# Kernel optimization log

Measured on AMD Instinct MI355X. Metric: run time of the kernel, lower is better.

The kernel has to match this reference:

```python
import jax, jax.numpy as jnp
import numpy as np

B, L, D_IN = 4, 2048, 80
D, H, DFF, WIN = 128, 16, 128, 64
DH = D // H
BN_EPS = 1e-5


def sinusoidal_positional_encoding(l, d, dtype):
    # Faithful to source: pos_j = 10000 ** (j / d) (exponent j/d, not 2j/d)
    n = d // 2 + (d % 2 == 1)
    pos_i = jnp.arange(l, dtype=dtype)[:, None]                  # [L,1]
    pos_j = jnp.power(jnp.asarray(10000.0, dtype), jnp.arange(n, dtype=dtype) / d)  # [n]
    ang = pos_i / pos_j                                          # [L,n]
    pos = jnp.stack([jnp.sin(ang), jnp.cos(ang)], axis=-1).reshape(l, -1)
    return pos[:, :d]                                            # [L,D]


def local_window_disallowed_mask(l, win):
    # Source: mask starts as ones (True = disallowed), zeros only strictly
    i = jnp.arange(l)
    diff = jnp.abs(i[:, None] - i[None, :])
    allowed = (diff >= 1) & (diff <= win)
    return ~allowed                                              # [L,L] bool, True = masked


def setup_inputs() -> dict:
    key = jax.random.key(0)
    ks = jax.random.split(key, 17)
    s = 0.05  # weight scale for numerical stability
    return {
        "x": jax.random.normal(ks[0], (B, L, D_IN), jnp.float32),
        "conv_w": jax.random.normal(ks[1], (D, D_IN), jnp.float32) * s,
        "conv_b": jax.random.normal(ks[2], (D,), jnp.float32) * s,
        "bn_g": jax.random.uniform(ks[3], (D,), jnp.float32, 0.5, 1.5),
        "bn_b": jax.random.normal(ks[4], (D,), jnp.float32) * s,
        "bn_rm": jax.random.normal(ks[5], (D,), jnp.float32) * s,
        "bn_rv": jax.random.uniform(ks[6], (D,), jnp.float32, 0.5, 1.5),
        "in_proj_w": jax.random.normal(ks[7], (3 * D, D), jnp.float32) * s,
        "in_proj_b": jax.random.normal(ks[8], (3 * D,), jnp.float32) * s,
        "out_w": jax.random.normal(ks[9], (D, D), jnp.float32) * s,
        "out_b": jax.random.normal(ks[10], (D,), jnp.float32) * s,
        "ff_w1": jax.random.normal(ks[11], (DFF, D), jnp.float32) * s,
        "ff_b1": jax.random.normal(ks[12], (DFF,), jnp.float32) * s,
        "ff_w2": jax.random.normal(ks[13], (D, DFF), jnp.float32) * s,
        "ff_b2": jax.random.normal(ks[14], (D,), jnp.float32) * s,
        "fc_w": jax.random.normal(ks[15], (D_IN, D), jnp.float32) * s,
        "fc_b": jax.random.normal(ks[16], (D_IN,), jnp.float32) * s,
    }


def _forward(x, conv_w, conv_b, bn_g, bn_b, bn_rm, bn_rv,
             in_proj_w, in_proj_b, out_w, out_b,
             ff_w1, ff_b1, ff_w2, ff_b2, fc_w, fc_b):
    b, l, _ = x.shape
    dt = x.dtype
    # Conv1d(kernel=1) + ReLU + BatchNorm1d (eval mode, running stats)
    h = jax.nn.relu(jnp.einsum('bli,oi->blo', x, conv_w) + conv_b)     # [B,L,D]
    h = (h - bn_rm) * (bn_g * jax.lax.rsqrt(bn_rv + BN_EPS)) + bn_b
    # positional encoding
    h = h + sinusoidal_positional_encoding(l, D, dt)
    # MultiheadAttention (torch semantics: joint in_proj, scaled dot, out_proj)
    qkv = jnp.einsum('bld,ed->ble', h, in_proj_w) + in_proj_b          # [B,L,3D]
    q, k, v = jnp.split(qkv, 3, axis=-1)
    q = q.reshape(b, l, H, DH).transpose(0, 2, 1, 3)                   # [B,H,L,dh]
    k = k.reshape(b, l, H, DH).transpose(0, 2, 1, 3)
    v = v.reshape(b, l, H, DH).transpose(0, 2, 1, 3)
    scores = jnp.einsum('bhqd,bhkd->bhqk', q, k) / jnp.sqrt(jnp.asarray(DH, dt))
    mask = local_window_disallowed_mask(l, WIN)                        # True = masked
    scores = jnp.where(mask, jnp.finfo(dt).min, scores)
    attn = jax.nn.softmax(scores, axis=-1)                             # [B,H,L,L]
    ctx = jnp.einsum('bhqk,bhkd->bhqd', attn, v)
    ctx = ctx.transpose(0, 2, 1, 3).reshape(b, l, D)
    attn_out = jnp.einsum('bld,od->blo', ctx, out_w) + out_b           # [B,L,D]
    # FFN (no residual in source)
    f = jax.nn.relu(jnp.einsum('bld,fd->blf', attn_out, ff_w1) + ff_b1)
    f = jnp.einsum('blf,df->bld', f, ff_w2) + ff_b2                    # [B,L,D]
    # final head
    return jnp.einsum('bld,od->blo', f, fc_w) + fc_b                   # [B,L,80]


def reference(x, conv_w, conv_b, bn_g, bn_b, bn_rm, bn_rv,
              in_proj_w, in_proj_b, out_w, out_b,
              ff_w1, ff_b1, ff_w2, ff_b2, fc_w, fc_b):
    return _forward(x, conv_w, conv_b, bn_g, bn_b, bn_rm, bn_rv,
                    in_proj_w, in_proj_b, out_w, out_b,
                    ff_w1, ff_b1, ff_w2, ff_b2, fc_w, fc_b)
```

## Files before the change

kernel.cpp:

```cpp
#include <hip/hip_runtime.h>
#include <math.h>

constexpr int B_ = 4, L_ = 2048, DIN = 80, D_ = 128, H_ = 16, DH = 8;
constexpr int T_ = B_ * L_;
constexpr int LDX = T_;

__device__ float g_xT  [DIN * T_];
__device__ float g_posT[D_ * L_];
__device__ float g_h   [D_ * T_];
__device__ float g_qkv [3 * D_ * T_];
__device__ float g_ctx [D_ * T_];
__device__ float g_f1  [D_ * T_];
__device__ float g_WconvT[DIN * D_];
__device__ float g_WqkvT [D_ * 3 * D_];
__device__ float g_Wf1T  [D_ * D_];
__device__ float g_WfcT  [D_ * D_];
__device__ float g_bf1   [D_];
__device__ float g_bfc   [D_];

__global__ __launch_bounds__(256) void prep_kernel(
        const float* __restrict__ x,
        const float* __restrict__ conv_w,
        const float* __restrict__ in_proj_w,
        const float* __restrict__ out_w,  const float* __restrict__ out_b,
        const float* __restrict__ ff_w1,  const float* __restrict__ ff_b1,
        const float* __restrict__ ff_w2,  const float* __restrict__ ff_b2,
        const float* __restrict__ fc_w,   const float* __restrict__ fc_b) {
    __shared__ float smem[80 * 65];
    int bid = blockIdx.x, tid = threadIdx.x;

    if (bid < 128) {
        int t0 = bid * 64;
        for (int i = tid; i < 64 * 80; i += 256) {
            int t = i / 80, k = i - t * 80;
            smem[k * 65 + t] = x[(size_t)t0 * 80 + i];
        }
        __syncthreads();
        for (int i = tid; i < 80 * 64; i += 256) {
            int k = i >> 6, tt = i & 63;
            g_xT[(size_t)k * T_ + t0 + tt] = smem[k * 65 + tt];
        }
        return;
    }
    if (bid < 640) {
        int idx = (bid - 128) * 256 + tid;
        int l = idx >> 6, j = idx & 63;
        float inv = __expf((float)j * (-9.210340371976184f / 128.0f));
        float ang = (float)l * inv;
        g_posT[(2 * j) * L_ + l]     = sinf(ang);
        g_posT[(2 * j + 1) * L_ + l] = cosf(ang);
        return;
    }
    if (bid < 680) {
        int e = (bid - 640) * 256 + tid;
        int o = e / 80, k = e - o * 80;
        g_WconvT[k * D_ + o] = conv_w[e];
        return;
    }
    if (bid < 872) {
        int e = (bid - 680) * 256 + tid;
        int o = e >> 7, k = e & 127;
        g_WqkvT[k * (3 * D_) + o] = in_proj_w[e];
        return;
    }
    float* rowbuf = smem;
    float* red = smem + 256;
    if (bid < 936) {
        int sub = tid >> 7, k = tid & 127;
        int f = (bid - 872) * 2 + sub;
        rowbuf[sub * 128 + k] = ff_w1[f * 128 + k];
        __syncthreads();
        float acc = 0.f;
#pragma unroll 8
        for (int o = 0; o < 128; o++)
            acc = fmaf(rowbuf[sub * 128 + o], out_w[o * 128 + k], acc);
        g_Wf1T[k * 128 + f] = acc;
        red[tid] = rowbuf[sub * 128 + k] * out_b[k];
        __syncthreads();
        for (int s = 64; s > 0; s >>= 1) {
            if (k < s) red[tid] += red[tid + s];
            __syncthreads();
        }
        if (k == 0) g_bf1[f] = red[sub * 128] + ff_b1[f];
        return;
    }
    {
        int sub = tid >> 7, k = tid & 127;
        int o = (bid - 936) * 2 + sub;
        rowbuf[sub * 128 + k] = (o < 80) ? fc_w[o * 128 + k] : 0.f;
        __syncthreads();
        float acc = 0.f;
#pragma unroll 8
        for (int d = 0; d < 128; d++)
            acc = fmaf(rowbuf[sub * 128 + d], ff_w2[d * 128 + k], acc);
        g_WfcT[k * 128 + o] = acc;
        red[tid] = rowbuf[sub * 128 + k] * ff_b2[k];
        __syncthreads();
        for (int s = 64; s > 0; s >>= 1) {
            if (k < s) red[tid] += red[tid + s];
            __syncthreads();
        }
        if (k == 0) g_bfc[o] = (o < 80) ? (red[sub * 128] + fc_b[o]) : 0.f;
        return;
    }
}

template <int K, int BK, int BN, int LDW, int EPI>
__global__ __launch_bounds__(256) void gemm_kernel(
        const float* __restrict__ X, const float* __restrict__ Wt,
        const float* __restrict__ bias,
        const float* __restrict__ bg, const float* __restrict__ bb,
        const float* __restrict__ brm, const float* __restrict__ brv,
        float* __restrict__ Y) {
    constexpr int TN = BN / 16;
    __shared__ float Xs[BK][64];
    __shared__ float Ws[BK][BN];
    int tid = threadIdx.x;
    int t0 = blockIdx.x * 64;
    int cb = blockIdx.y * BN;
    int tc = tid & 15, tr = tid >> 4;

    float acc[4][TN] = {};
    for (int kc = 0; kc < K; kc += BK) {
        for (int i = tid; i < BK * 16; i += 256) {
            int k = i >> 4, f = i & 15;
            *(float4*)&Xs[k][f * 4] =
                *(const float4*)&X[(size_t)(kc + k) * LDX + t0 + f * 4];
        }
        for (int i = tid; i < BK * (BN / 4); i += 256) {
            int k = i / (BN / 4), f = i - k * (BN / 4);
            *(float4*)&Ws[k][f * 4] =
                *(const float4*)&Wt[(size_t)(kc + k) * LDW + cb + f * 4];
        }
        __syncthreads();
#pragma unroll 4
        for (int k = 0; k < BK; ++k) {
            float4 a = *(float4*)&Xs[k][tr * 4];
            float av[4] = {a.x, a.y, a.z, a.w};
            float wv[TN];
#pragma unroll
            for (int jj = 0; jj < TN; jj++) wv[jj] = Ws[k][tc * TN + jj];
#pragma unroll
            for (int i = 0; i < 4; i++)
#pragma unroll
                for (int jj = 0; jj < TN; jj++)
                    acc[i][jj] = fmaf(av[i], wv[jj], acc[i][jj]);
        }
        __syncthreads();
    }

    if (EPI == 4) {
#pragma unroll
        for (int jj = 0; jj < TN; jj++) {
            int c = cb + tc * TN + jj;
            if (c < 80) {
                float bv = bias[c];
#pragma unroll
                for (int i = 0; i < 4; i++) {
                    int t = t0 + tr * 4 + i;
                    Y[(size_t)t * 80 + c] = acc[i][jj] + bv;
                }
            }
        }
        return;
    }
#pragma unroll
    for (int jj = 0; jj < TN; jj++) {
        int c = cb + tc * TN + jj;
        float bv = bias[c];
        float vs[4];
#pragma unroll
        for (int i = 0; i < 4; i++) {
            float v = acc[i][jj] + bv;
            if (EPI == 1) v = fmaxf(v, 0.0f);
            if (EPI == 2) {
                v = fmaxf(v, 0.0f);
                v = (v - brm[c]) * (bg[c] * rsqrtf(brv[c] + 1e-5f)) + bb[c];
                v += g_posT[c * L_ + ((t0 & 2047) + tr * 4 + i)];
            }
            vs[i] = v;
        }
        *(float4*)&Y[(size_t)c * LDX + t0 + tr * 4] = *(float4*)vs;
    }
}

__global__ __launch_bounds__(256) void attn_kernel() {
    __shared__ float4 SK[2][2][324];
    __shared__ float4 SV[2][2][324];
    int bh = blockIdx.x;
    int qb = blockIdx.y * 512;
    int b = bh >> 4, h = bh & 15;
    int tb = b * L_;
    int tid = threadIdx.x;
    int jbase = qb - 64;

    for (int c16 = 0; c16 < 16; c16++) {
        int d = c16 & 7;
        int ch = ((c16 < 8) ? D_ : 2 * D_) + h * 8 + d;
        const float* src = g_qkv + (size_t)ch * LDX + tb;
        float4* base4 = ((c16 < 8) ? &SK[0][0][0] : &SV[0][0][0]) + (d >> 2) * 324;
        for (int s = tid; s < 641; s += 256) {
            int j = jbase + s;
            float v = ((unsigned)j < (unsigned)L_) ? src[j] : 0.f;
            ((float*)(base4 + (s & 1) * 648 + (s >> 1)))[d & 3] = v;
        }
    }
    __syncthreads();

    const float sc = 0.35355339059327373f;
    int q0 = qb + 2 * tid;
    float qa[8], qc[8];
#pragma unroll
    for (int d = 0; d < 8; d++) {
        qa[d] = g_qkv[(size_t)(h * 8 + d) * LDX + tb + q0] * sc;
        qc[d] = g_qkv[(size_t)(h * 8 + d) * LDX + tb + q0 + 1] * sc;
    }
    float l0 = 0.f, l1 = 0.f;
    float A0[8] = {}, A1[8] = {};
    int j00 = jbase + 2 * tid;

#pragma unroll 2
    for (int it = 0; it <= 129; it++) {
        int pp = it & 1, idx = tid + (it >> 1);
        float4 ka = SK[pp][0][idx], kb2 = SK[pp][1][idx];
        float kv[8] = {ka.x, ka.y, ka.z, ka.w, kb2.x, kb2.y, kb2.z, kb2.w};
        float s0 = 0.f, s1 = 0.f;
#pragma unroll
        for (int d = 0; d < 8; d++) {
            s0 = fmaf(qa[d], kv[d], s0);
            s1 = fmaf(qc[d], kv[d], s1);
        }
        bool jv = (unsigned)(j00 + it) < (unsigned)L_;
        float w0 = (jv && it != 64 && it <= 128) ? __expf(s0) : 0.f;
        float w1 = (jv && it != 65 && it >= 1)  ? __expf(s1) : 0.f;
        l0 += w0; l1 += w1;
        float4 va = SV[pp][0][idx], vb2 = SV[pp][1][idx];
        float vv[8] = {va.x, va.y, va.z, va.w, vb2.x, vb2.y, vb2.z, vb2.w};
#pragma unroll
        for (int d = 0; d < 8; d++) {
            A0[d] = fmaf(w0, vv[d], A0[d]);
            A1[d] = fmaf(w1, vv[d], A1[d]);
        }
    }
    float i0 = 1.f / l0, i1 = 1.f / l1;
    int base = tb + q0;
#pragma unroll
    for (int d = 0; d < 8; d++) {
        g_ctx[(size_t)(h * 8 + d) * LDX + base]     = A0[d] * i0;
        g_ctx[(size_t)(h * 8 + d) * LDX + base + 1] = A1[d] * i1;
    }
}

extern "C" void kernel_launch(void* const* d_in, const int* in_sizes, int n_in,
                              void* d_out, int out_size, void* d_ws, size_t ws_size,
                              hipStream_t stream) {
    const float* x         = (const float*)d_in[0];
    const float* conv_w    = (const float*)d_in[1];
    const float* conv_b    = (const float*)d_in[2];
    const float* bn_g      = (const float*)d_in[3];
    const float* bn_b      = (const float*)d_in[4];
    const float* bn_rm     = (const float*)d_in[5];
    const float* bn_rv     = (const float*)d_in[6];
    const float* in_proj_w = (const float*)d_in[7];
    const float* in_proj_b = (const float*)d_in[8];
    const float* out_w     = (const float*)d_in[9];
    const float* out_b     = (const float*)d_in[10];
    const float* ff_w1     = (const float*)d_in[11];
    const float* ff_b1     = (const float*)d_in[12];
    const float* ff_w2     = (const float*)d_in[13];
    const float* ff_b2     = (const float*)d_in[14];
    const float* fc_w      = (const float*)d_in[15];
    const float* fc_b      = (const float*)d_in[16];

    float *p_xT, *p_h, *p_qkv, *p_ctx, *p_f1;
    float *p_WconvT, *p_WqkvT, *p_Wf1T, *p_WfcT, *p_bf1, *p_bfc;
    hipGetSymbolAddress((void**)&p_xT,     HIP_SYMBOL(g_xT));
    hipGetSymbolAddress((void**)&p_h,      HIP_SYMBOL(g_h));
    hipGetSymbolAddress((void**)&p_qkv,    HIP_SYMBOL(g_qkv));
    hipGetSymbolAddress((void**)&p_ctx,    HIP_SYMBOL(g_ctx));
    hipGetSymbolAddress((void**)&p_f1,     HIP_SYMBOL(g_f1));
    hipGetSymbolAddress((void**)&p_WconvT, HIP_SYMBOL(g_WconvT));
    hipGetSymbolAddress((void**)&p_WqkvT,  HIP_SYMBOL(g_WqkvT));
    hipGetSymbolAddress((void**)&p_Wf1T,   HIP_SYMBOL(g_Wf1T));
    hipGetSymbolAddress((void**)&p_WfcT,   HIP_SYMBOL(g_WfcT));
    hipGetSymbolAddress((void**)&p_bf1,    HIP_SYMBOL(g_bf1));
    hipGetSymbolAddress((void**)&p_bfc,    HIP_SYMBOL(g_bfc));

    prep_kernel<<<1000, 256, 0, stream>>>(x, conv_w, in_proj_w, out_w, out_b,
                                          ff_w1, ff_b1, ff_w2, ff_b2, fc_w, fc_b);

    gemm_kernel<80, 80, 32, 128, 2><<<dim3(128, 4), 256, 0, stream>>>(
        p_xT, p_WconvT, conv_b, bn_g, bn_b, bn_rm, bn_rv, p_h);

    gemm_kernel<128, 64, 64, 384, 0><<<dim3(128, 6), 256, 0, stream>>>(
        p_h, p_WqkvT, in_proj_b, nullptr, nullptr, nullptr, nullptr, p_qkv);

    attn_kernel<<<dim3(64, 4), 256, 0, stream>>>();

    gemm_kernel<128, 128, 32, 128, 1><<<dim3(128, 4), 256, 0, stream>>>(
        p_ctx, p_Wf1T, p_bf1, nullptr, nullptr, nullptr, nullptr, p_f1);

    gemm_kernel<128, 128, 32, 128, 4><<<dim3(128, 3), 256, 0, stream>>>(
        p_f1, p_WfcT, p_bfc, nullptr, nullptr, nullptr, nullptr, (float*)d_out);
}
```

Baseline: 167.6 us.

## Fuse FFN and output head GEMMs, add dedicated QKV kernel

Merges the two final GEMMs (ff1 with ReLU, then the fc head) into one kernel that keeps the intermediate activations in shared memory, so the g_f1 buffer is never written to or read back from global memory. The QKV projection moves to a specialised kernel with an 8x4 per-thread tile and vectorised weight loads. The conv GEMM tile width doubles to 64 so it launches half as many blocks, and the shared weight read becomes a float4 load when TN is 4. The fused kernel launches only 256 blocks with heavy shared-memory use, which may limit occupancy.

```diff
diff --git a/kernel.cpp b/kernel.cpp
--- a/kernel.cpp
+++ b/kernel.cpp
@@ -1,8 +1,9 @@
 #include <hip/hip_runtime.h>
 #include <math.h>
 
-constexpr int B_ = 4, L_ = 2048, DIN = 80, D_ = 128, H_ = 16, DH = 8;
-constexpr int T_ = B_ * L_;
+constexpr int L_ = 2048, D_ = 128, H_ = 16;
+constexpr int T_ = 8192;
+constexpr int DIN = 80;
 constexpr int LDX = T_;
 
 __device__ float g_xT  [DIN * T_];
@@ -10,7 +11,6 @@
 __device__ float g_h   [D_ * T_];
 __device__ float g_qkv [3 * D_ * T_];
 __device__ float g_ctx [D_ * T_];
-__device__ float g_f1  [D_ * T_];
 __device__ float g_WconvT[DIN * D_];
 __device__ float g_WqkvT [D_ * 3 * D_];
 __device__ float g_Wf1T  [D_ * D_];
@@ -138,8 +138,13 @@
             float4 a = *(float4*)&Xs[k][tr * 4];
             float av[4] = {a.x, a.y, a.z, a.w};
             float wv[TN];
-#pragma unroll
-            for (int jj = 0; jj < TN; jj++) wv[jj] = Ws[k][tc * TN + jj];
+            if (TN == 4) {
+                float4 w = *(float4*)&Ws[k][tc * 4];
+                wv[0] = w.x; wv[1] = w.y; wv[2] = w.z; wv[3] = w.w;
+            } else {
+#pragma unroll
+                for (int jj = 0; jj < TN; jj++) wv[jj] = Ws[k][tc * TN + jj];
+            }
 #pragma unroll
             for (int i = 0; i < 4; i++)
 #pragma unroll
@@ -149,21 +154,6 @@
         __syncthreads();
     }
 
-    if (EPI == 4) {
-#pragma unroll
-        for (int jj = 0; jj < TN; jj++) {
-            int c = cb + tc * TN + jj;
-            if (c < 80) {
-                float bv = bias[c];
-#pragma unroll
-                for (int i = 0; i < 4; i++) {
-                    int t = t0 + tr * 4 + i;
-                    Y[(size_t)t * 80 + c] = acc[i][jj] + bv;
-                }
-            }
-        }
-        return;
-    }
 #pragma unroll
     for (int jj = 0; jj < TN; jj++) {
         int c = cb + tc * TN + jj;
@@ -184,6 +174,55 @@
     }
 }
 
+__global__ __launch_bounds__(256) void qkv_kernel(const float* __restrict__ in_proj_b) {
+    __shared__ float Xs[64 * 128];
+    __shared__ float Ws[64 * 64];
+    int tid = threadIdx.x;
+    int t0 = blockIdx.x * 128;
+    int cb = blockIdx.y * 64;
+    int tc = tid & 15, tr = tid >> 4;
+
+    float acc[8][4] = {};
+    for (int kc = 0; kc < 128; kc += 64) {
+        for (int i = tid; i < 64 * 32; i += 256) {
+            int k = i >> 5, f = i & 31;
+            *(float4*)&Xs[k * 128 + f * 4] =
+                *(const float4*)&g_h[(size_t)(kc + k) * LDX + t0 + f * 4];
+        }
+        for (int i = tid; i < 64 * 16; i += 256) {
+            int k = i >> 4, f = i & 15;
+            *(float4*)&Ws[k * 64 + f * 4] =
+                *(const float4*)&g_WqkvT[(size_t)(kc + k) * 384 + cb + f * 4];
+        }
+        __syncthreads();
+#pragma unroll 4
+        for (int k = 0; k < 64; k++) {
+            float4 a0 = *(float4*)&Xs[k * 128 + tr * 8];
+            float4 a1 = *(float4*)&Xs[k * 128 + tr * 8 + 4];
+            float4 w  = *(float4*)&Ws[k * 64 + tc * 4];
+            float av[8] = {a0.x, a0.y, a0.z, a0.w, a1.x, a1.y, a1.z, a1.w};
+            float wv[4] = {w.x, w.y, w.z, w.w};
+#pragma unroll
+            for (int i = 0; i < 8; i++)
+#pragma unroll
+                for (int jj = 0; jj < 4; jj++)
+                    acc[i][jj] = fmaf(av[i], wv[jj], acc[i][jj]);
+        }
+        __syncthreads();
+    }
+
+#pragma unroll
+    for (int jj = 0; jj < 4; jj++) {
+        int C = cb + tc * 4 + jj;
+        float bv = in_proj_b[C];
+        float vs[8];
+#pragma unroll
+        for (int i = 0; i < 8; i++) vs[i] = acc[i][jj] + bv;
+        *(float4*)&g_qkv[(size_t)C * LDX + t0 + tr * 8]     = *(float4*)&vs[0];
+        *(float4*)&g_qkv[(size_t)C * LDX + t0 + tr * 8 + 4] = *(float4*)&vs[4];
+    }
+}
+
 __global__ __launch_bounds__(256) void attn_kernel() {
     __shared__ float4 SK[2][2][324];
     __shared__ float4 SV[2][2][324];
@@ -248,6 +287,86 @@
     for (int d = 0; d < 8; d++) {
         g_ctx[(size_t)(h * 8 + d) * LDX + base]     = A0[d] * i0;
         g_ctx[(size_t)(h * 8 + d) * LDX + base + 1] = A1[d] * i1;
+    }
+}
+
+__global__ __launch_bounds__(256) void f1fc_kernel(float* __restrict__ out) {
+    __shared__ float Xs[128 * 32];
+    __shared__ float Wsh[32 * 128];
+    __shared__ float F[128 * 36];
+    int tid = threadIdx.x;
+    int t0 = blockIdx.x * 32;
+    int tc = tid & 31, tr = tid >> 5;
+
+    for (int i = tid; i < 128 * 8; i += 256) {
+        int k = i >> 3, f = i & 7;
+        *(float4*)&Xs[k * 32 + f * 4] =
+            *(const float4*)&g_ctx[(size_t)k * LDX + t0 + f * 4];
+    }
+
+    float acc[4][4] = {};
+    for (int kc = 0; kc < 128; kc += 32) {
+        for (int i = tid; i < 32 * 32; i += 256) {
+            int k = i >> 5, f = i & 31;
+            *(float4*)&Wsh[k * 128 + f * 4] =
+                *(const float4*)&g_Wf1T[(size_t)(kc + k) * 128 + f * 4];
+        }
+        __syncthreads();
+#pragma unroll 4
+        for (int k = 0; k < 32; k++) {
+            float4 a = *(float4*)&Xs[(kc + k) * 32 + tr * 4];
+            float4 w = *(float4*)&Wsh[k * 128 + tc * 4];
+            float av[4] = {a.x, a.y, a.z, a.w};
+            float wv[4] = {w.x, w.y, w.z, w.w};
+#pragma unroll
+            for (int i = 0; i < 4; i++)
+#pragma unroll
+                for (int jj = 0; jj < 4; jj++)
+                    acc[i][jj] = fmaf(av[i], wv[jj], acc[i][jj]);
+        }
+        __syncthreads();
+    }
+#pragma unroll
+    for (int jj = 0; jj < 4; jj++) {
+        int c = tc * 4 + jj;
+        float bv = g_bf1[c];
+#pragma unroll
+        for (int i = 0; i < 4; i++)
+            F[c * 36 + tr * 4 + i] = fmaxf(acc[i][jj] + bv, 0.f);
+    }
+    __syncthreads();
+
+    float acc2[4][4] = {};
+    for (int kc = 0; kc < 128; kc += 32) {
+        for (int i = tid; i < 32 * 32; i += 256) {
+            int k = i >> 5, f = i & 31;
+            *(float4*)&Wsh[k * 128 + f * 4] =
+                *(const float4*)&g_WfcT[(size_t)(kc + k) * 128 + f * 4];
+        }
+        __syncthreads();
+#pragma unroll 4
+        for (int k = 0; k < 32; k++) {
+            float4 a = *(float4*)&F[(kc + k) * 36 + tr * 4];
+            float4 w = *(float4*)&Wsh[k * 128 + tc * 4];
+            float av[4] = {a.x, a.y, a.z, a.w};
+            float wv[4] = {w.x, w.y, w.z, w.w};
+#pragma unroll
+            for (int i = 0; i < 4; i++)
+#pragma unroll
+                for (int jj = 0; jj < 4; jj++)
+                    acc2[i][jj] = fmaf(av[i], wv[jj], acc2[i][jj]);
+        }
+        __syncthreads();
+    }
+    if (tc < 20) {
+#pragma unroll
+        for (int i = 0; i < 4; i++) {
+            int t = t0 + tr * 4 + i;
+            float vs[4];
+#pragma unroll
+            for (int jj = 0; jj < 4; jj++) vs[jj] = acc2[i][jj] + g_bfc[tc * 4 + jj];
+            *(float4*)&out[(size_t)t * 80 + tc * 4] = *(float4*)vs;
+        }
     }
 }
 
@@ -272,34 +391,20 @@
     const float* fc_w      = (const float*)d_in[15];
     const float* fc_b      = (const float*)d_in[16];
 
-    float *p_xT, *p_h, *p_qkv, *p_ctx, *p_f1;
-    float *p_WconvT, *p_WqkvT, *p_Wf1T, *p_WfcT, *p_bf1, *p_bfc;
+    float *p_xT, *p_h, *p_WconvT;
     hipGetSymbolAddress((void**)&p_xT,     HIP_SYMBOL(g_xT));
     hipGetSymbolAddress((void**)&p_h,      HIP_SYMBOL(g_h));
-    hipGetSymbolAddress((void**)&p_qkv,    HIP_SYMBOL(g_qkv));
-    hipGetSymbolAddress((void**)&p_ctx,    HIP_SYMBOL(g_ctx));
-    hipGetSymbolAddress((void**)&p_f1,     HIP_SYMBOL(g_f1));
     hipGetSymbolAddress((void**)&p_WconvT, HIP_SYMBOL(g_WconvT));
-    hipGetSymbolAddress((void**)&p_WqkvT,  HIP_SYMBOL(g_WqkvT));
-    hipGetSymbolAddress((void**)&p_Wf1T,   HIP_SYMBOL(g_Wf1T));
-    hipGetSymbolAddress((void**)&p_WfcT,   HIP_SYMBOL(g_WfcT));
-    hipGetSymbolAddress((void**)&p_bf1,    HIP_SYMBOL(g_bf1));
-    hipGetSymbolAddress((void**)&p_bfc,    HIP_SYMBOL(g_bfc));
 
     prep_kernel<<<1000, 256, 0, stream>>>(x, conv_w, in_proj_w, out_w, out_b,
                                           ff_w1, ff_b1, ff_w2, ff_b2, fc_w, fc_b);
 
-    gemm_kernel<80, 80, 32, 128, 2><<<dim3(128, 4), 256, 0, stream>>>(
+    gemm_kernel<80, 80, 64, 128, 2><<<dim3(128, 2), 256, 0, stream>>>(
         p_xT, p_WconvT, conv_b, bn_g, bn_b, bn_rm, bn_rv, p_h);
 
-    gemm_kernel<128, 64, 64, 384, 0><<<dim3(128, 6), 256, 0, stream>>>(
-        p_h, p_WqkvT, in_proj_b, nullptr, nullptr, nullptr, nullptr, p_qkv);
+    qkv_kernel<<<dim3(64, 6), 256, 0, stream>>>(in_proj_b);
 
     attn_kernel<<<dim3(64, 4), 256, 0, stream>>>();
 
-    gemm_kernel<128, 128, 32, 128, 1><<<dim3(128, 4), 256, 0, stream>>>(
-        p_ctx, p_Wf1T, p_bf1, nullptr, nullptr, nullptr, nullptr, p_f1);
-
-    gemm_kernel<128, 128, 32, 128, 4><<<dim3(128, 3), 256, 0, stream>>>(
-        p_f1, p_WfcT, p_bfc, nullptr, nullptr, nullptr, nullptr, (float*)d_out);
-}
+    f1fc_kernel<<<256, 256, 0, stream>>>((float*)d_out);
+}
```

Result: slower. 177.8 us (+6.1%).
